# Kernel tuning notes

Hardware: AMD Instinct MI355X
Metric: run time of the kernel (lower is better)

Reference implementation:

```python
import jax, jax.numpy as jnp
import numpy as np
from jax import lax

B, C, L = 8, 256, 2048
DK, DV, KS = 256, 256, 3
PAD = (KS - 1) // 2  # odd kernel -> dilation 1, same-length padding


def conv1d(x, w, b):
    # x: (B, C, L), w: (O, C, KS), b: (O,)
    y = lax.conv_general_dilated(
        x, w, window_strides=(1,), padding=[(PAD, PAD)],
        rhs_dilation=(1,), dimension_numbers=("NCH", "OIH", "NCH"))
    return y + b[None, :, None]


def setup_inputs() -> dict:
    key = jax.random.key(0)
    ks = jax.random.split(key, 7)
    sc = 1.0 / np.sqrt(C * KS)
    return {
        "x": jax.random.normal(ks[0], (B, C, L), dtype=jnp.float32),
        "Wq": jax.random.normal(ks[1], (DK, C, KS), dtype=jnp.float32) * sc,
        "bq": jnp.zeros((DK,), dtype=jnp.float32),
        "Wk": jax.random.normal(ks[2], (DK, C, KS), dtype=jnp.float32) * sc,
        "bk": jnp.zeros((DK,), dtype=jnp.float32),
        "Wv": jax.random.normal(ks[3], (DV, C, KS), dtype=jnp.float32) * sc,
        "bv": jnp.zeros((DV,), dtype=jnp.float32),
    }


def reference(x, Wq, bq, Wk, bk, Wv, bv):
    Q = conv1d(x, Wq, bq)  # (B, DK, L)
    K = conv1d(x, Wk, bk)  # (B, DK, L)
    V = conv1d(x, Wv, bv)  # (B, DV, L)
    # A = softmax(Q^T K / sqrt(dk)) over key axis
    scores = jnp.einsum("bdq,bdk->bqk", Q, K) / jnp.sqrt(jnp.float32(DK))
    A = jax.nn.softmax(scores, axis=2)  # (B, L, L)
    H = jnp.einsum("bqk,bdk->bdq", A, V)  # (B, DV, L)
    return H
```

## Files before the change

kernel.cpp:

```cpp
#include <hip/hip_runtime.h>
#include <hip/hip_bf16.h>
#include <stdint.h>


typedef __bf16 bf16;
typedef __bf16 bf16x2 __attribute__((ext_vector_type(2)));
typedef __bf16 bf16x4 __attribute__((ext_vector_type(4)));
typedef __bf16 bf16x8 __attribute__((ext_vector_type(8)));
typedef float f32x4 __attribute__((ext_vector_type(4)));
typedef uint32_t u32x4 __attribute__((ext_vector_type(4)));
typedef __attribute__((address_space(1))) const uint32_t cu32_as1;
typedef __attribute__((address_space(3))) uint32_t u32_as3;

#define DEVI __device__ __forceinline__
#define LOG2E 1.44269504088896f

DEVI void async_copy16(const void* g, void* l) {
  __builtin_amdgcn_global_load_lds((cu32_as1*)g, (u32_as3*)l, 16, 0, 0);
}

DEVI void block_sync() {
  asm volatile("" ::: "memory");
  __builtin_amdgcn_s_barrier();
  asm volatile("" ::: "memory");
}

#define VMCNT(n) asm volatile("s_waitcnt vmcnt(" #n ")" ::: "memory")

__global__ void prep_w(const float* __restrict__ Wq, const float* __restrict__ Wk,
                       const float* __restrict__ Wv, const float* __restrict__ bq,
                       const float* __restrict__ bk, const float* __restrict__ bv,
                       bf16* __restrict__ W2, float* __restrict__ biasA) {
  const float QSC = 0.0625f * LOG2E;
  int idx = blockIdx.x * 256 + threadIdx.x;
  if (idx < 768 * 768) {
    int o = idx / 768, kk = idx - o * 768;
    int ks = kk >> 8, c = kk & 255;
    const float* W = (o < 256) ? Wq : ((o < 512) ? Wk : Wv);
    int ol = o & 255;
    float w = W[ol * 768 + c * 3 + ks];
    if (o < 256) w *= QSC;
    W2[o * 768 + kk] = (bf16)w;
  }
  if (idx < 768) {
    float v;
    if (idx < 256) v = bq[idx] * QSC;
    else if (idx < 512) v = bk[idx - 256];
    else v = bv[idx - 512];
    biasA[idx] = v;
  }
}

__global__ void prep_x(const float* __restrict__ x, bf16* __restrict__ xT) {
  __shared__ float tile[32][33];
  int bid = blockIdx.x;
  int lt = bid & 63, ct = (bid >> 6) & 7, b = bid >> 9;
  int t = threadIdx.x;
  int tl = t & 31, tc = t >> 5;
  const float* xb = x + (size_t)b * 256 * 2048;
#pragma unroll
  for (int i = 0; i < 4; ++i) {
    int c = ct * 32 + tc + i * 8;
    tile[tc + i * 8][tl] = xb[(size_t)c * 2048 + lt * 32 + tl];
  }
  __syncthreads();
  bf16* xTb = xT + (size_t)b * 2050 * 256;
#pragma unroll
  for (int i = 0; i < 4; ++i) {
    int l = lt * 32 + tc + i * 8;
    xTb[(size_t)(l + 1) * 256 + ct * 32 + tl] = (bf16)tile[tl][tc + i * 8];
  }
  if (lt == 0 && t < 32) xTb[ct * 32 + t] = (bf16)0.f;
  if (lt == 63 && t < 32) xTb[(size_t)2049 * 256 + ct * 32 + t] = (bf16)0.f;
}

__launch_bounds__(256, 2)
__global__ void conv_gemm(const bf16* __restrict__ W2, const bf16* __restrict__ xT,
                          const float* __restrict__ biasA, bf16* __restrict__ QT,
                          bf16* __restrict__ KT, bf16* __restrict__ V) {
  __shared__ bf16 Alds[128 * 64];
  __shared__ bf16 Blds[128 * 64];
  const int t = threadIdx.x;
  const int w = t >> 6, lane = t & 63;
  const int g = lane >> 4, lr = lane & 15;
  const int wr = w >> 1, wc = w & 1;
  const int bid = blockIdx.x;
  const int b = bid & 7;
  const int rest = bid >> 3;
  const int ot = rest % 6;
  const int lt = rest / 6;
  const int l0 = lt * 128;

  const bf16* xTb = xT + (size_t)b * 2050 * 256;
  const bf16* Ab = W2 + (size_t)(ot * 128) * 768;

  const int srow = t >> 3;
  const int scb = ((t & 7) * 16) ^ ((srow & 7) << 4);

  f32x4 acc[4][4];
#pragma unroll
  for (int i = 0; i < 4; ++i)
#pragma unroll
    for (int j = 0; j < 4; ++j) acc[i][j] = (f32x4){0.f, 0.f, 0.f, 0.f};

  for (int step = 0; step < 12; ++step) {
    const int kk = step * 64;
    const int ks = kk >> 8;
    const int c0 = kk & 255;
    const bf16* As = Ab + kk + (scb >> 1);
    const bf16* Bs = xTb + (size_t)(l0 + ks) * 256 + c0 + (scb >> 1);
#pragma unroll
    for (int i = 0; i < 4; ++i) {
      const int row = srow + i * 32;
      async_copy16(As + (size_t)row * 768, (char*)Alds + w * 1024 + i * 4096);
      async_copy16(Bs + (size_t)row * 256, (char*)Blds + w * 1024 + i * 4096);
    }
    asm volatile("s_waitcnt vmcnt(0)" ::: "memory");
    __syncthreads();
#pragma unroll
    for (int sub = 0; sub < 2; ++sub) {
      bf16x8 af[4], bfr[4];
#pragma unroll
      for (int mf = 0; mf < 4; ++mf) {
        const int row = wr * 64 + mf * 16 + lr;
        const int cb = (sub * 64 + g * 16) ^ ((row & 7) << 4);
        af[mf] = *(const bf16x8*)((const char*)Alds + row * 128 + cb);
      }
#pragma unroll
      for (int nf = 0; nf < 4; ++nf) {
        const int row = wc * 64 + nf * 16 + lr;
        const int cb = (sub * 64 + g * 16) ^ ((row & 7) << 4);
        bfr[nf] = *(const bf16x8*)((const char*)Blds + row * 128 + cb);
      }
#pragma unroll
      for (int mf = 0; mf < 4; ++mf)
#pragma unroll
        for (int nf = 0; nf < 4; ++nf)
          acc[mf][nf] = __builtin_amdgcn_mfma_f32_16x16x32_bf16(af[mf], bfr[nf], acc[mf][nf], 0, 0, 0);
    }
    __syncthreads();
  }

  const int obase = ot * 128 + wr * 64;
  const int lbase = l0 + wc * 64;
  if (ot < 4) {
    bf16* dst = ((ot < 2) ? QT : KT) + (size_t)b * 2048 * 256;
#pragma unroll
    for (int mf = 0; mf < 4; ++mf) {
      const int og = obase + mf * 16 + g * 4;
      float bb[4];
#pragma unroll
      for (int r = 0; r < 4; ++r) bb[r] = biasA[og + r];
#pragma unroll
      for (int nf = 0; nf < 4; ++nf) {
        const int l = lbase + nf * 16 + lr;
        bf16x4 pk;
#pragma unroll
        for (int r = 0; r < 4; ++r) pk[r] = (bf16)(acc[mf][nf][r] + bb[r]);
        *(bf16x4*)(dst + (size_t)l * 256 + (og & 255)) = pk;
      }
    }
  } else {
    bf16* dst = V + (size_t)b * 256 * 2048;
#pragma unroll
    for (int mf = 0; mf < 4; ++mf) {
      const int og = obase + mf * 16 + g * 4;
      float bb[4];
#pragma unroll
      for (int r = 0; r < 4; ++r) bb[r] = biasA[og + r];
      const int ov = og - 512;
#pragma unroll
      for (int nf = 0; nf < 4; ++nf) {
        const int l = lbase + nf * 16 + lr;
#pragma unroll
        for (int r = 0; r < 4; ++r)
          dst[(size_t)(ov + r) * 2048 + l] = (bf16)(acc[mf][nf][r] + bb[r]);
      }
    }
  }
}

__launch_bounds__(256, 2)
__global__ void attn(const bf16* __restrict__ QT, const bf16* __restrict__ KT,
                     const bf16* __restrict__ V, bf16* __restrict__ Opart,
                     float* __restrict__ Sl) {
  __shared__ bf16 Klds[2 * 32 * 256];
  __shared__ bf16 Vlds[128 * 64];
  const int t = threadIdx.x;
  const int w = t >> 6, lane = t & 63;
  const int g = lane >> 4, lr = lane & 15;
  const int bid = blockIdx.x;
  const int b = bid & 7;
  const int kvh = (bid >> 3) & 3;
  const int qt = bid >> 5;
  const int q0w = qt * 128 + w * 32;
  const int kb0 = kvh * 512;
  const bf16* QTb = QT + (size_t)b * 2048 * 256;
  const bf16* KTb = KT + (size_t)b * 2048 * 256;
  const bf16* Vb = V + (size_t)b * 256 * 2048;

  auto stageK = [&](int kt, int p) {
#pragma unroll
    for (int i = 0; i < 4; ++i) {
      const int row = i * 8 + (t >> 5);
      const int col = ((t & 31) ^ row) * 8;
      const bf16* src = KTb + (size_t)(kb0 + kt * 32 + row) * 256 + col;
      async_copy16(src, (char*)Klds + p * 16384 + i * 4096 + t * 16);
    }
  };
  auto stageV = [&](int kt) {
#pragma unroll
    for (int i = 0; i < 4; ++i) {
      const int row = i * 32 + (t >> 3);
      const int ls = (t & 7) ^ (row & 7);
      const int d = row * 2 + (ls >> 2);
      const int k0 = (ls & 3) * 8;
      const bf16* src = Vb + (size_t)d * 2048 + kb0 + kt * 32 + k0;
      async_copy16(src, (char*)Vlds + i * 4096 + t * 16);
    }
  };

  bf16x8 qreg[2][8];
#pragma unroll
  for (int qfr = 0; qfr < 2; ++qfr)
#pragma unroll
    for (int ds = 0; ds < 8; ++ds)
      qreg[qfr][ds] = *(const bf16x8*)(QTb + (size_t)(q0w + qfr * 16 + lr) * 256 + ds * 32 + g * 8);

  f32x4 oacc[16][2];
#pragma unroll
  for (int i = 0; i < 16; ++i) {
    oacc[i][0] = (f32x4){0.f, 0.f, 0.f, 0.f};
    oacc[i][1] = (f32x4){0.f, 0.f, 0.f, 0.f};
  }
  float l_acc[2] = {0.f, 0.f};

  stageV(0);
  stageK(0, 0);
  stageK(1, 1);

  for (int kt = 0; kt < 16; ++kt) {
    const int p = kt & 1;
    if (kt == 15) { VMCNT(0); } else { VMCNT(4); }
    block_sync();

    f32x4 sT[2][2];
#pragma unroll
    for (int kfr = 0; kfr < 2; ++kfr)
#pragma unroll
      for (int qfr = 0; qfr < 2; ++qfr) sT[kfr][qfr] = (f32x4){0.f, 0.f, 0.f, 0.f};
#pragma unroll
    for (int ds = 0; ds < 8; ++ds) {
      bf16x8 kf[2];
#pragma unroll
      for (int kfr = 0; kfr < 2; ++kfr) {
        const int row = kfr * 16 + lr;
        kf[kfr] = *(const bf16x8*)((const char*)Klds + p * 16384 + row * 512 +
                                   (((ds * 4 + g) ^ row) * 16));
      }
#pragma unroll
      for (int kfr = 0; kfr < 2; ++kfr)
#pragma unroll
        for (int qfr = 0; qfr < 2; ++qfr)
          sT[kfr][qfr] = __builtin_amdgcn_mfma_f32_16x16x32_bf16(kf[kfr], qreg[qfr][ds], sT[kfr][qfr], 0, 0, 0);
    }

#pragma unroll
    for (int kfr = 0; kfr < 2; ++kfr)
#pragma unroll
      for (int qfr = 0; qfr < 2; ++qfr)
#pragma unroll
        for (int r = 0; r < 4; ++r) {
          float pe = __builtin_exp2f(sT[kfr][qfr][r]);
          sT[kfr][qfr][r] = pe;
          l_acc[qfr] += pe;
        }

    bf16x8 pB[2];
#pragma unroll
    for (int qfr = 0; qfr < 2; ++qfr) {
      uint32_t wq[2][2];
#pragma unroll
      for (int kfr = 0; kfr < 2; ++kfr)
#pragma unroll
        for (int pp = 0; pp < 2; ++pp) {
          bf16x2 pr;
          pr[0] = (bf16)sT[kfr][qfr][2 * pp];
          pr[1] = (bf16)sT[kfr][qfr][2 * pp + 1];
          wq[kfr][pp] = __builtin_bit_cast(uint32_t, pr);
        }
      uint32_t bw[4];
#pragma unroll
      for (int j = 0; j < 4; ++j) {
        const int srcLane = ((g & 1) * 2 + (j >> 1)) * 16 + lr;
        const uint32_t a = (uint32_t)__shfl((int)wq[0][j & 1], srcLane, 64);
        const uint32_t bb = (uint32_t)__shfl((int)wq[1][j & 1], srcLane, 64);
        bw[j] = (lane < 32) ? a : bb;
      }
      u32x4 v4 = {bw[0], bw[1], bw[2], bw[3]};
      pB[qfr] = __builtin_bit_cast(bf16x8, v4);
    }

#pragma unroll
    for (int dfr = 0; dfr < 16; ++dfr) {
      const int row = dfr * 8 + (lr >> 1);
      bf16x8 vf = *(const bf16x8*)((const char*)Vlds + row * 128 +
                                   ((((lr & 1) * 4 + g) ^ ((lr >> 1) & 7)) * 16));
      oacc[dfr][0] = __builtin_amdgcn_mfma_f32_16x16x32_bf16(vf, pB[0], oacc[dfr][0], 0, 0, 0);
      oacc[dfr][1] = __builtin_amdgcn_mfma_f32_16x16x32_bf16(vf, pB[1], oacc[dfr][1], 0, 0, 0);
    }
    block_sync();
    if (kt < 15) stageV(kt + 1);
    if (kt < 14) stageK(kt + 2, p);
  }

#pragma unroll
  for (int qfr = 0; qfr < 2; ++qfr) {
    float rv = l_acc[qfr];
    rv += __shfl_xor(rv, 16, 64);
    rv += __shfl_xor(rv, 32, 64);
    l_acc[qfr] = rv;
  }

  bf16* Op = Opart + (size_t)bid * 128 * 256;
#pragma unroll
  for (int qfr = 0; qfr < 2; ++qfr) {
    const int ql = w * 32 + qfr * 16 + lr;
#pragma unroll
    for (int dfr = 0; dfr < 16; ++dfr) {
      const int d0 = dfr * 16 + g * 4;
      bf16x4 pk;
#pragma unroll
      for (int r = 0; r < 4; ++r) pk[r] = (bf16)oacc[dfr][qfr][r];
      *(bf16x4*)(Op + (size_t)ql * 256 + d0) = pk;
    }
    if (g == 0) Sl[bid * 128 + ql] = l_acc[qfr];
  }
}

__launch_bounds__(256)
__global__ void merge_p(const bf16* __restrict__ Opart, const float* __restrict__ Sl,
                        float* __restrict__ H) {
  __shared__ float Ocomb[32][257];
  const int bid = blockIdx.x;
  const int b = bid & 7;
  const int qt = (bid >> 3) & 15;
  const int qc = bid >> 7;
  const int t = threadIdx.x;
  const int g2 = t >> 5, lane2 = t & 31;
  float* Hb = H + (size_t)b * 256 * 2048 + qt * 128 + qc * 32;

#pragma unroll
  for (int qb = 0; qb < 4; ++qb) {
    const int qq = qb * 8 + g2;
    const int ql = qc * 32 + qq;
    float wsum = 0.f;
    float o[8];
#pragma unroll
    for (int j = 0; j < 8; ++j) o[j] = 0.f;
#pragma unroll
    for (int kvh = 0; kvh < 4; ++kvh) {
      const int blk = b + 8 * kvh + 32 * qt;
      wsum += Sl[blk * 128 + ql];
      bf16x8 v = *(const bf16x8*)(Opart + ((size_t)blk * 128 + ql) * 256 + lane2 * 8);
#pragma unroll
      for (int j = 0; j < 8; ++j) o[j] += (float)v[j];
    }
    const float inv = 1.f / wsum;
#pragma unroll
    for (int j = 0; j < 8; ++j) Ocomb[qq][lane2 * 8 + j] = o[j] * inv;
  }
  __syncthreads();
  const int q = t & 31;
  const int dbase = (t >> 5) * 32;
#pragma unroll
  for (int j = 0; j < 32; ++j) {
    const int d = dbase + j;
    Hb[(size_t)d * 2048 + q] = Ocomb[q][d];
  }
}

extern "C" void kernel_launch(void* const* d_in, const int* in_sizes, int n_in,
                              void* d_out, int out_size, void* d_ws, size_t ws_size,
                              hipStream_t stream) {
  (void)in_sizes; (void)n_in; (void)out_size; (void)ws_size;
  const float* x = (const float*)d_in[0];
  const float* Wq = (const float*)d_in[1];
  const float* bq = (const float*)d_in[2];
  const float* Wk = (const float*)d_in[3];
  const float* bk = (const float*)d_in[4];
  const float* Wv = (const float*)d_in[5];
  const float* bv = (const float*)d_in[6];
  char* ws = (char*)d_ws;
  bf16* xT = (bf16*)(ws + 0);
  bf16* W2 = (bf16*)(ws + 8396800);
  float* biasA = (float*)(ws + 9576448);
  bf16* QT = (bf16*)(ws + 9580544);
  bf16* KT = (bf16*)(ws + 17969152);
  bf16* V = (bf16*)(ws + 26357760);
  bf16* Opart = (bf16*)(ws + 34746368);
  float* Sl = (float*)(ws + 68300800);
  float* H = (float*)d_out;

  prep_w<<<dim3(2304), dim3(256), 0, stream>>>(Wq, Wk, Wv, bq, bk, bv, W2, biasA);
  prep_x<<<dim3(4096), dim3(256), 0, stream>>>(x, xT);
  conv_gemm<<<dim3(768), dim3(256), 0, stream>>>(W2, xT, biasA, QT, KT, V);
  attn<<<dim3(512), dim3(256), 0, stream>>>(QT, KT, V, Opart, Sl);
  merge_p<<<dim3(512), dim3(256), 0, stream>>>(Opart, Sl, H);
}
```

Before: 113.3 us.

## Add MFMA priority hints, scheduler barriers, and wider transpose tiles in prep_x

Wraps the two MFMA loops in the attention kernel with s_setprio so waves in their matrix phase get issue priority over waves doing softmax or loads. Adds sched_barrier around the block barrier so the compiler cannot move instructions across it. Separately, prep_x now transposes 64-channel by 32-position tiles, so each row of bf16 stores covers 128 contiguous bytes and half as many blocks are launched. These are small independent scheduling and memory-coalescing tweaks. The sched barriers may limit the compiler's interleaving.

```diff
diff --git a/kernel.cpp b/kernel.cpp
--- a/kernel.cpp
+++ b/kernel.cpp
@@ -21,7 +21,9 @@
 
 DEVI void block_sync() {
   asm volatile("" ::: "memory");
+  __builtin_amdgcn_sched_barrier(0);
   __builtin_amdgcn_s_barrier();
+  __builtin_amdgcn_sched_barrier(0);
   asm volatile("" ::: "memory");
 }
 
@@ -52,26 +54,29 @@
 }
 
 __global__ void prep_x(const float* __restrict__ x, bf16* __restrict__ xT) {
-  __shared__ float tile[32][33];
-  int bid = blockIdx.x;
-  int lt = bid & 63, ct = (bid >> 6) & 7, b = bid >> 9;
-  int t = threadIdx.x;
-  int tl = t & 31, tc = t >> 5;
+  __shared__ float tile[64][33];
+  const int bid = blockIdx.x;
+  const int b = bid >> 8;
+  const int rest = bid & 255;
+  const int ct = rest & 3;
+  const int lt = rest >> 2;
+  const int c0 = ct * 64, l0 = lt * 32;
+  const int t = threadIdx.x;
   const float* xb = x + (size_t)b * 256 * 2048;
 #pragma unroll
-  for (int i = 0; i < 4; ++i) {
-    int c = ct * 32 + tc + i * 8;
-    tile[tc + i * 8][tl] = xb[(size_t)c * 2048 + lt * 32 + tl];
+  for (int i = 0; i < 8; ++i) {
+    const int cc = (t >> 5) + i * 8;
+    tile[cc][t & 31] = xb[(size_t)(c0 + cc) * 2048 + l0 + (t & 31)];
   }
   __syncthreads();
   bf16* xTb = xT + (size_t)b * 2050 * 256;
 #pragma unroll
-  for (int i = 0; i < 4; ++i) {
-    int l = lt * 32 + tc + i * 8;
-    xTb[(size_t)(l + 1) * 256 + ct * 32 + tl] = (bf16)tile[tl][tc + i * 8];
-  }
-  if (lt == 0 && t < 32) xTb[ct * 32 + t] = (bf16)0.f;
-  if (lt == 63 && t < 32) xTb[(size_t)2049 * 256 + ct * 32 + t] = (bf16)0.f;
+  for (int j = 0; j < 8; ++j) {
+    const int ll = (t >> 6) + j * 4;
+    xTb[(size_t)(l0 + ll + 1) * 256 + c0 + (t & 63)] = (bf16)tile[t & 63][ll];
+  }
+  if (lt == 0 && t < 64) xTb[c0 + t] = (bf16)0.f;
+  if (lt == 63 && t < 64) xTb[(size_t)2049 * 256 + c0 + t] = (bf16)0.f;
 }
 
 __launch_bounds__(256, 2)
@@ -249,6 +254,7 @@
     for (int kfr = 0; kfr < 2; ++kfr)
 #pragma unroll
       for (int qfr = 0; qfr < 2; ++qfr) sT[kfr][qfr] = (f32x4){0.f, 0.f, 0.f, 0.f};
+    __builtin_amdgcn_s_setprio(1);
 #pragma unroll
     for (int ds = 0; ds < 8; ++ds) {
       bf16x8 kf[2];
@@ -264,6 +270,7 @@
         for (int qfr = 0; qfr < 2; ++qfr)
           sT[kfr][qfr] = __builtin_amdgcn_mfma_f32_16x16x32_bf16(kf[kfr], qreg[qfr][ds], sT[kfr][qfr], 0, 0, 0);
     }
+    __builtin_amdgcn_s_setprio(0);
 
 #pragma unroll
     for (int kfr = 0; kfr < 2; ++kfr)
@@ -301,6 +308,7 @@
       pB[qfr] = __builtin_bit_cast(bf16x8, v4);
     }
 
+    __builtin_amdgcn_s_setprio(1);
 #pragma unroll
     for (int dfr = 0; dfr < 16; ++dfr) {
       const int row = dfr * 8 + (lr >> 1);
@@ -309,6 +317,7 @@
       oacc[dfr][0] = __builtin_amdgcn_mfma_f32_16x16x32_bf16(vf, pB[0], oacc[dfr][0], 0, 0, 0);
       oacc[dfr][1] = __builtin_amdgcn_mfma_f32_16x16x32_bf16(vf, pB[1], oacc[dfr][1], 0, 0, 0);
     }
+    __builtin_amdgcn_s_setprio(0);
     block_sync();
     if (kt < 15) stageV(kt + 1);
     if (kt < 14) stageK(kt + 2, p);
@@ -403,7 +412,7 @@
   float* H = (float*)d_out;
 
   prep_w<<<dim3(2304), dim3(256), 0, stream>>>(Wq, Wk, Wv, bq, bk, bv, W2, biasA);
-  prep_x<<<dim3(4096), dim3(256), 0, stream>>>(x, xT);
+  prep_x<<<dim3(2048), dim3(256), 0, stream>>>(x, xT);
   conv_gemm<<<dim3(768), dim3(256), 0, stream>>>(W2, xT, biasA, QT, KT, V);
   attn<<<dim3(512), dim3(256), 0, stream>>>(QT, KT, V, Opart, Sl);
   merge_p<<<dim3(512), dim3(256), 0, stream>>>(Opart, Sl, H);
```

New measurement: 108.7 us. -4.0%, faster.
